# Performance work log

Measured on AMD Instinct MI355X. Metric: run time of the kernel, lower is better.

The kernel has to match this reference:

```python
import jax, jax.numpy as jnp
import numpy as np

N_NODES = 50000
N_EDGES = 800000
H_DIM = 64
N_RELS = 8
N_BASES = 2
N_LAYERS = 2


def setup_inputs() -> dict:
    key = jax.random.key(0)
    ks = jax.random.split(key, 10)
    scale = 1.0 / np.sqrt(H_DIM)
    features = jax.random.normal(ks[0], (N_NODES, H_DIM), dtype=jnp.float32)
    src = jax.random.randint(ks[1], (N_EDGES,), 0, N_NODES, dtype=jnp.int32)
    dst = jax.random.randint(ks[2], (N_EDGES,), 0, N_NODES, dtype=jnp.int32)
    etype = jax.random.randint(ks[3], (N_EDGES,), 0, N_RELS, dtype=jnp.int32)
    # basis weights V: [L, B, H, H], coefficients comp: [L, R, B]
    V = jax.random.normal(ks[4], (N_LAYERS, N_BASES, H_DIM, H_DIM), dtype=jnp.float32) * scale
    comp = jax.random.normal(ks[5], (N_LAYERS, N_RELS, N_BASES), dtype=jnp.float32)
    loop_w = jax.random.normal(ks[6], (N_LAYERS, H_DIM, H_DIM), dtype=jnp.float32) * scale
    layer_bias = jnp.zeros((N_LAYERS, H_DIM), dtype=jnp.float32)
    fc_w = jax.random.normal(ks[7], (1, N_NODES * H_DIM), dtype=jnp.float32) * (1.0 / np.sqrt(N_NODES * H_DIM))
    fc_b = jnp.zeros((1,), dtype=jnp.float32)
    return {
        "features": features, "V": V, "comp": comp, "loop_w": loop_w,
        "layer_bias": layer_bias, "fc_w": fc_w, "fc_b": fc_b,
        "src": src, "dst": dst, "etype": etype,
    }


def reference(features, V, comp, loop_w, layer_bias, fc_w, fc_b, src, dst, etype):
    N, H = features.shape
    L = V.shape[0]
    x = features
    for l in range(L):
        # basis decomposition: project nodes through each basis first (N*B*H, cheap),
        # then mix per-edge with relation coefficients -> avoids per-edge [H,H] weights
        proj = jnp.einsum('ni,bio->nbo', x, V[l])          # [N, B, H]
        msg = jnp.einsum('eb,ebo->eo', comp[l][etype], proj[src])  # [E, H]
        agg = jax.ops.segment_sum(msg, dst, num_segments=N)        # [N, H]
        h = agg + x @ loop_w[l] + layer_bias[l]
        x = jax.nn.relu(h) if l < L - 1 else h
    flat = x.reshape(1, -1)                                # [1, N*H]
    return jax.nn.sigmoid(flat @ fc_w.T + fc_b)            # [1, 1]
```

## Files before the change

### kernel.cpp

```cpp
#include <hip/hip_runtime.h>
#include <hip/hip_bf16.h>
#include <math.h>

#define N_NODES 50000
#define N_EDGES 800000
#define HDIM 64

#define NBUCKET 392
#define BSHIFT  7
#define NLOC    128
#define BCAP    3072

typedef short bf16x8 __attribute__((ext_vector_type(8)));
typedef float f32x4  __attribute__((ext_vector_type(4)));
typedef unsigned short ushort_t;

__device__ __forceinline__ ushort_t f2bf(float f) {
    __hip_bfloat16 b = __float2bfloat16(f);
    return *(ushort_t*)&b;
}
__device__ __forceinline__ void unpack8(uint4 u, float* f) {
    f[0] = __uint_as_float(u.x << 16); f[1] = __uint_as_float(u.x & 0xFFFF0000u);
    f[2] = __uint_as_float(u.y << 16); f[3] = __uint_as_float(u.y & 0xFFFF0000u);
    f[4] = __uint_as_float(u.z << 16); f[5] = __uint_as_float(u.z & 0xFFFF0000u);
    f[6] = __uint_as_float(u.w << 16); f[7] = __uint_as_float(u.w & 0xFFFF0000u);
}

__global__ __launch_bounds__(256) void prep_kernel(
    const float* __restrict__ features, ushort_t* __restrict__ x_bf,
    const float* __restrict__ V, const float* __restrict__ lw,
    ushort_t* __restrict__ Wt, int* __restrict__ bucketFill,
    float* __restrict__ scalar, int* __restrict__ done)
{
    const int b = blockIdx.x;
    const int t = threadIdx.x;
    if (b < 3125) {
        const int i = b * 256 + t;
        const float4 v = ((const float4*)features)[i];
        ushort4 o = { f2bf(v.x), f2bf(v.y), f2bf(v.z), f2bf(v.w) };
        *(ushort4*)&x_bf[(size_t)i * 4] = o;
    } else if (b < 3221) {
        const int e = (b - 3125) * 256 + t;
        const int l = e / 12288, r = e % 12288;
        const int n = r / 192, k = r % 192;
        const int sel = k >> 6, i = k & 63;
        const float val = (sel < 2) ? V[l * 8192 + sel * 4096 + i * 64 + n]
                                    : lw[l * 4096 + i * 64 + n];
        Wt[e] = f2bf(val);
    } else {
        for (int i = t; i < NBUCKET; i += 256) bucketFill[i] = 0;
        if (t == 0) { scalar[0] = 0.0f; done[0] = 0; }
    }
}

__global__ __launch_bounds__(256) void bucket_scatter(
    const int* __restrict__ src, const int* __restrict__ dst,
    const int* __restrict__ etype, int* __restrict__ bucketFill,
    unsigned int* __restrict__ buf)
{
    __shared__ int cnt[NBUCKET];
    __shared__ int base[NBUCKET];
    const int t = threadIdx.x;
    for (int i = t; i < NBUCKET; i += 256) cnt[i] = 0;
    __syncthreads();

    int rank[8], bkt[8];
    unsigned pay[8];
    bool valid[8];
#pragma unroll
    for (int k = 0; k < 8; ++k) {
        const int e = blockIdx.x * 2048 + k * 256 + t;
        valid[k] = (e < N_EDGES);
        if (valid[k]) {
            const int d = dst[e];
            const int b = d >> BSHIFT;
            bkt[k] = b;
            pay[k] = (unsigned)src[e] | ((unsigned)etype[e] << 16)
                   | ((unsigned)(d & (NLOC - 1)) << 19);
            rank[k] = atomicAdd(&cnt[b], 1);
        }
    }
    __syncthreads();
    for (int i = t; i < NBUCKET; i += 256)
        base[i] = atomicAdd(&bucketFill[i], cnt[i]);
    __syncthreads();
#pragma unroll
    for (int k = 0; k < 8; ++k) {
        if (valid[k]) {
            const int pos = base[bkt[k]] + rank[k];
            if (pos < BCAP) buf[bkt[k] * BCAP + pos] = pay[k];
        }
    }
}

__global__ __launch_bounds__(256) void bucket_sort(
    const unsigned int* __restrict__ buf, const int* __restrict__ bucketFill,
    unsigned int* __restrict__ edges, int* __restrict__ row_ptr)
{
    __shared__ int hist[NLOC];
    __shared__ int lscan[NLOC];
    __shared__ int cnt2[NLOC];
    __shared__ int sraw[448];
    __shared__ int sexc[448];
    const int b = blockIdx.x;
    const int t = threadIdx.x;

    if (t < NLOC) { hist[t] = 0; cnt2[t] = 0; }
    for (int i = t; i < 448; i += 256)
        sraw[i] = (i < NBUCKET) ? bucketFill[i] : 0;
    __syncthreads();

    if (t < 64) {
        int carry = 0;
        for (int c = 0; c < 7; ++c) {
            const int h = sraw[c * 64 + t];
            int x = h;
#pragma unroll
            for (int off = 1; off < 64; off <<= 1) {
                int u = __shfl_up(x, off, 64);
                if (t >= off) x += u;
            }
            sexc[c * 64 + t] = carry + x - h;
            carry += __shfl(x, 63, 64);
        }
    }
    __syncthreads();
    const int cntb = min(sraw[b], BCAP);
    const int bb   = sexc[b];

    for (int i0 = t; i0 < cntb; i0 += 1024) {
        const bool v1 = i0 + 256 < cntb, v2 = i0 + 512 < cntb, v3 = i0 + 768 < cntb;
        const unsigned p0 = buf[b * BCAP + i0];
        unsigned p1 = 0, p2 = 0, p3 = 0;
        if (v1) p1 = buf[b * BCAP + i0 + 256];
        if (v2) p2 = buf[b * BCAP + i0 + 512];
        if (v3) p3 = buf[b * BCAP + i0 + 768];
        atomicAdd(&hist[p0 >> 19], 1);
        if (v1) atomicAdd(&hist[p1 >> 19], 1);
        if (v2) atomicAdd(&hist[p2 >> 19], 1);
        if (v3) atomicAdd(&hist[p3 >> 19], 1);
    }
    __syncthreads();

    if (t < 64) {
        int carry = 0;
        for (int c = 0; c < 2; ++c) {
            const int h = hist[c * 64 + t];
            int x = h;
#pragma unroll
            for (int off = 1; off < 64; off <<= 1) {
                int u = __shfl_up(x, off, 64);
                if (t >= off) x += u;
            }
            lscan[c * 64 + t] = carry + x - h;
            carry += __shfl(x, 63, 64);
        }
    }
    __syncthreads();

    const int n0 = b << BSHIFT;
    if (t < NLOC) {
        const int g = n0 + t;
        if (g < N_NODES) row_ptr[g] = bb + lscan[t];
    }
    if (b == NBUCKET - 1 && t == 0) row_ptr[N_NODES] = bb + cntb;

    for (int i0 = t; i0 < cntb; i0 += 1024) {
        const bool v1 = i0 + 256 < cntb, v2 = i0 + 512 < cntb, v3 = i0 + 768 < cntb;
        const unsigned p0 = buf[b * BCAP + i0];
        unsigned p1 = 0, p2 = 0, p3 = 0;
        if (v1) p1 = buf[b * BCAP + i0 + 256];
        if (v2) p2 = buf[b * BCAP + i0 + 512];
        if (v3) p3 = buf[b * BCAP + i0 + 768];
        {
            const int d = p0 >> 19;
            const int r = atomicAdd(&cnt2[d], 1);
            edges[bb + lscan[d] + r] = p0 & 0x7FFFFu;
        }
        if (v1) { const int d = p1 >> 19; const int r = atomicAdd(&cnt2[d], 1);
                  edges[bb + lscan[d] + r] = p1 & 0x7FFFFu; }
        if (v2) { const int d = p2 >> 19; const int r = atomicAdd(&cnt2[d], 1);
                  edges[bb + lscan[d] + r] = p2 & 0x7FFFFu; }
        if (v3) { const int d = p3 >> 19; const int r = atomicAdd(&cnt2[d], 1);
                  edges[bb + lscan[d] + r] = p3 & 0x7FFFFu; }
    }
}

template <bool FUSE>
__global__ __launch_bounds__(256) void fused_layer(
    const ushort_t* __restrict__ xin,
    const unsigned int* __restrict__ edges,
    const int* __restrict__ row_ptr,
    const float* __restrict__ comp_l,
    const ushort_t* __restrict__ Wt,
    const float* __restrict__ bias,
    const float* __restrict__ fcw,
    ushort_t* __restrict__ xout,
    float* __restrict__ scalar,
    const float* __restrict__ fcb,
    int* __restrict__ done,
    float* __restrict__ outp)
{
    __shared__ __align__(16) ushort_t su[32 * 200];
    __shared__ float sred[4];
    const int t = threadIdx.x;
    const int tile = blockIdx.x;

    const int grp = t >> 3;
    const int fo  = t & 7;
    const int n   = tile * 32 + grp;

    int beg = 0, end = 0;
    if (n < N_NODES) { beg = row_ptr[n]; end = row_ptr[n + 1]; }

    float a0[8], a1[8];
#pragma unroll
    for (int i = 0; i < 8; ++i) { a0[i] = 0.f; a1[i] = 0.f; }

    for (int j = beg; j < end; j += 4) {
        unsigned pk[4];
        float2 c[4];
#pragma unroll
        for (int k = 0; k < 4; ++k) {
            const int jk = j + k;
            const unsigned p = edges[(jk < end) ? jk : (end - 1)];
            pk[k] = p;
            float2 cc = *(const float2*)&comp_l[(p >> 16) * 2];
            if (jk >= end) { cc.x = 0.f; cc.y = 0.f; }
            c[k] = cc;
        }
        uint4 u[4];
#pragma unroll
        for (int k = 0; k < 4; ++k)
            u[k] = *(const uint4*)&xin[(size_t)(pk[k] & 0xFFFFu) * 64 + fo * 8];
#pragma unroll
        for (int k = 0; k < 4; ++k) {
            float f[8];
            unpack8(u[k], f);
#pragma unroll
            for (int i = 0; i < 8; ++i) {
                a0[i] = fmaf(c[k].x, f[i], a0[i]);
                a1[i] = fmaf(c[k].y, f[i], a1[i]);
            }
        }
    }

    uint4 o0, o1;
    o0.x = (unsigned)f2bf(a0[0]) | ((unsigned)f2bf(a0[1]) << 16);
    o0.y = (unsigned)f2bf(a0[2]) | ((unsigned)f2bf(a0[3]) << 16);
    o0.z = (unsigned)f2bf(a0[4]) | ((unsigned)f2bf(a0[5]) << 16);
    o0.w = (unsigned)f2bf(a0[6]) | ((unsigned)f2bf(a0[7]) << 16);
    o1.x = (unsigned)f2bf(a1[0]) | ((unsigned)f2bf(a1[1]) << 16);
    o1.y = (unsigned)f2bf(a1[2]) | ((unsigned)f2bf(a1[3]) << 16);
    o1.z = (unsigned)f2bf(a1[4]) | ((unsigned)f2bf(a1[5]) << 16);
    o1.w = (unsigned)f2bf(a1[6]) | ((unsigned)f2bf(a1[7]) << 16);
    uint4 xt = {0u, 0u, 0u, 0u};
    if (n < N_NODES) xt = *(const uint4*)&xin[(size_t)n * 64 + fo * 8];
    *(uint4*)&su[grp * 200 + fo * 8]        = o0;
    *(uint4*)&su[grp * 200 + (8 + fo) * 8]  = o1;
    *(uint4*)&su[grp * 200 + (16 + fo) * 8] = xt;
    __syncthreads();

    const int w    = t >> 6;
    const int lane = t & 63;
    const int c16  = lane & 15;
    const int quad = lane >> 4;

    bf16x8 wf[6];
#pragma unroll
    for (int kf = 0; kf < 6; ++kf)
        wf[kf] = *(const bf16x8*)&Wt[(w * 16 + c16) * 192 + kf * 32 + quad * 8];
    const float bv = bias[w * 16 + c16];

    float fsum = 0.f;
#pragma unroll
    for (int mt = 0; mt < 2; ++mt) {
        f32x4 acc = {bv, bv, bv, bv};
#pragma unroll
        for (int kf = 0; kf < 6; ++kf) {
            const bf16x8 af =
                *(const bf16x8*)&su[(mt * 16 + c16) * 200 + kf * 32 + quad * 8];
            acc = __builtin_amdgcn_mfma_f32_16x16x32_bf16(af, wf[kf], acc, 0, 0, 0);
        }
        const int nodeb = tile * 32 + mt * 16 + quad * 4;
        if (FUSE) {
#pragma unroll
            for (int r = 0; r < 4; ++r) {
                const int nn = nodeb + r;
                if (nn < N_NODES)
                    fsum += acc[r] * fcw[(size_t)nn * 64 + w * 16 + c16];
            }
        } else {
#pragma unroll
            for (int r = 0; r < 4; ++r) {
                const int nn = nodeb + r;
                if (nn < N_NODES)
                    xout[(size_t)nn * 64 + w * 16 + c16] = f2bf(fmaxf(acc[r], 0.f));
            }
        }
    }

    if (FUSE) {
#pragma unroll
        for (int off = 32; off; off >>= 1) fsum += __shfl_down(fsum, off, 64);
        if (lane == 0) sred[w] = fsum;
        __syncthreads();
        if (t == 0) {
            atomicAdd(scalar, sred[0] + sred[1] + sred[2] + sred[3]);
            __threadfence();
            const int ticket = atomicAdd(done, 1);
            if (ticket == (int)gridDim.x - 1) {
                const float v = atomicAdd(scalar, 0.0f) + fcb[0];
                outp[0] = 1.0f / (1.0f + expf(-v));
            }
        }
    }
}

extern "C" void kernel_launch(void* const* d_in, const int* in_sizes, int n_in,
                              void* d_out, int out_size, void* d_ws, size_t ws_size,
                              hipStream_t stream)
{
    const float* features = (const float*)d_in[0];
    const float* V        = (const float*)d_in[1];
    const float* comp     = (const float*)d_in[2];
    const float* loop_w   = (const float*)d_in[3];
    const float* bias     = (const float*)d_in[4];
    const float* fc_w     = (const float*)d_in[5];
    const float* fc_b     = (const float*)d_in[6];
    const int*   src      = (const int*)d_in[7];
    const int*   dst      = (const int*)d_in[8];
    const int*   etype    = (const int*)d_in[9];
    float* out = (float*)d_out;

    char* ws = (char*)d_ws;
    ushort_t*     x_bf    = (ushort_t*)(ws);
    ushort_t*     x1_bf   = (ushort_t*)(ws + 6400000);
    ushort_t*     Wt      = (ushort_t*)(ws + 12800000);
    float*        scalar  = (float*)   (ws + 12849152);
    int*          done    = (int*)     (ws + 12849156);
    int*          bucketFill = (int*)  (ws + 12849280);
    int*          row_ptr = (int*)     (ws + 12850944);
    unsigned int* edges   = (unsigned int*)(ws + 13051008);
    unsigned int* buf     = (unsigned int*)(ws + 16251008);

    const int flBlocks = (N_NODES + 31) / 32;
    const int k1Blocks = (N_EDGES + 2047) / 2048;

    prep_kernel<<<3222, 256, 0, stream>>>(features, x_bf, V, loop_w, Wt,
                                          bucketFill, scalar, done);
    bucket_scatter<<<k1Blocks, 256, 0, stream>>>(src, dst, etype, bucketFill, buf);
    bucket_sort<<<NBUCKET, 256, 0, stream>>>(buf, bucketFill, edges, row_ptr);

    fused_layer<false><<<flBlocks, 256, 0, stream>>>(
        x_bf, edges, row_ptr, comp, Wt, bias, nullptr, x1_bf,
        nullptr, nullptr, nullptr, nullptr);

    fused_layer<true><<<flBlocks, 256, 0, stream>>>(
        x1_bf, edges, row_ptr, comp + 16, Wt + 12288, bias + 64, fc_w, nullptr,
        scalar, fc_b, done, out);
}
```

Measured before the change: 206.3 us.

## Aggregate edges per tile with wave-per-edge LDS float atomics instead of per-node loops

Replaces the per-node gather, where 8 threads walk one node's edge list, with a tile-wide edge loop. Each wave takes groups of 4 edges, each lane loads one feature, and partial sums are accumulated into an fp32 LDS buffer with atomics, using a fast path when all 4 edges share a destination. Edge records now keep the destination bits so the local slot can be recovered. This is meant to remove load imbalance from varying node degree and the serialized per-node loops. In exchange it uses scalar 2-byte loads and LDS atomic traffic, and needs extra LDS and an extra sync.

New measurement: 594.2 us. 2.88x slower.

```diff
diff --git a/kernel.cpp b/kernel.cpp
--- a/kernel.cpp
+++ b/kernel.cpp
@@ -18,12 +18,6 @@
 __device__ __forceinline__ ushort_t f2bf(float f) {
     __hip_bfloat16 b = __float2bfloat16(f);
     return *(ushort_t*)&b;
-}
-__device__ __forceinline__ void unpack8(uint4 u, float* f) {
-    f[0] = __uint_as_float(u.x << 16); f[1] = __uint_as_float(u.x & 0xFFFF0000u);
-    f[2] = __uint_as_float(u.y << 16); f[3] = __uint_as_float(u.y & 0xFFFF0000u);
-    f[4] = __uint_as_float(u.z << 16); f[5] = __uint_as_float(u.z & 0xFFFF0000u);
-    f[6] = __uint_as_float(u.w << 16); f[7] = __uint_as_float(u.w & 0xFFFF0000u);
 }
 
 __global__ __launch_bounds__(256) void prep_kernel(
@@ -175,14 +169,14 @@
         {
             const int d = p0 >> 19;
             const int r = atomicAdd(&cnt2[d], 1);
-            edges[bb + lscan[d] + r] = p0 & 0x7FFFFu;
+            edges[bb + lscan[d] + r] = p0;
         }
         if (v1) { const int d = p1 >> 19; const int r = atomicAdd(&cnt2[d], 1);
-                  edges[bb + lscan[d] + r] = p1 & 0x7FFFFu; }
+                  edges[bb + lscan[d] + r] = p1; }
         if (v2) { const int d = p2 >> 19; const int r = atomicAdd(&cnt2[d], 1);
-                  edges[bb + lscan[d] + r] = p2 & 0x7FFFFu; }
+                  edges[bb + lscan[d] + r] = p2; }
         if (v3) { const int d = p3 >> 19; const int r = atomicAdd(&cnt2[d], 1);
-                  edges[bb + lscan[d] + r] = p3 & 0x7FFFFu; }
+                  edges[bb + lscan[d] + r] = p3; }
     }
 }
 
@@ -201,76 +195,98 @@
     int* __restrict__ done,
     float* __restrict__ outp)
 {
+    __shared__ __align__(16) float    suf[32 * 128];
     __shared__ __align__(16) ushort_t su[32 * 200];
     __shared__ float sred[4];
-    const int t = threadIdx.x;
+    const int t    = threadIdx.x;
     const int tile = blockIdx.x;
-
-    const int grp = t >> 3;
-    const int fo  = t & 7;
-    const int n   = tile * 32 + grp;
-
-    int beg = 0, end = 0;
-    if (n < N_NODES) { beg = row_ptr[n]; end = row_ptr[n + 1]; }
-
-    float a0[8], a1[8];
-#pragma unroll
-    for (int i = 0; i < 8; ++i) { a0[i] = 0.f; a1[i] = 0.f; }
-
-    for (int j = beg; j < end; j += 4) {
-        unsigned pk[4];
-        float2 c[4];
-#pragma unroll
-        for (int k = 0; k < 4; ++k) {
-            const int jk = j + k;
-            const unsigned p = edges[(jk < end) ? jk : (end - 1)];
-            pk[k] = p;
-            float2 cc = *(const float2*)&comp_l[(p >> 16) * 2];
-            if (jk >= end) { cc.x = 0.f; cc.y = 0.f; }
-            c[k] = cc;
-        }
-        uint4 u[4];
-#pragma unroll
-        for (int k = 0; k < 4; ++k)
-            u[k] = *(const uint4*)&xin[(size_t)(pk[k] & 0xFFFFu) * 64 + fo * 8];
-#pragma unroll
-        for (int k = 0; k < 4; ++k) {
-            float f[8];
-            unpack8(u[k], f);
-#pragma unroll
-            for (int i = 0; i < 8; ++i) {
-                a0[i] = fmaf(c[k].x, f[i], a0[i]);
-                a1[i] = fmaf(c[k].y, f[i], a1[i]);
-            }
-        }
-    }
-
-    uint4 o0, o1;
-    o0.x = (unsigned)f2bf(a0[0]) | ((unsigned)f2bf(a0[1]) << 16);
-    o0.y = (unsigned)f2bf(a0[2]) | ((unsigned)f2bf(a0[3]) << 16);
-    o0.z = (unsigned)f2bf(a0[4]) | ((unsigned)f2bf(a0[5]) << 16);
-    o0.w = (unsigned)f2bf(a0[6]) | ((unsigned)f2bf(a0[7]) << 16);
-    o1.x = (unsigned)f2bf(a1[0]) | ((unsigned)f2bf(a1[1]) << 16);
-    o1.y = (unsigned)f2bf(a1[2]) | ((unsigned)f2bf(a1[3]) << 16);
-    o1.z = (unsigned)f2bf(a1[4]) | ((unsigned)f2bf(a1[5]) << 16);
-    o1.w = (unsigned)f2bf(a1[6]) | ((unsigned)f2bf(a1[7]) << 16);
-    uint4 xt = {0u, 0u, 0u, 0u};
-    if (n < N_NODES) xt = *(const uint4*)&xin[(size_t)n * 64 + fo * 8];
-    *(uint4*)&su[grp * 200 + fo * 8]        = o0;
-    *(uint4*)&su[grp * 200 + (8 + fo) * 8]  = o1;
-    *(uint4*)&su[grp * 200 + (16 + fo) * 8] = xt;
-    __syncthreads();
-
     const int w    = t >> 6;
     const int lane = t & 63;
     const int c16  = lane & 15;
     const int quad = lane >> 4;
+    const int grp  = t >> 3;
+    const int fo   = t & 7;
 
     bf16x8 wf[6];
 #pragma unroll
     for (int kf = 0; kf < 6; ++kf)
         wf[kf] = *(const bf16x8*)&Wt[(w * 16 + c16) * 192 + kf * 32 + quad * 8];
     const float bv = bias[w * 16 + c16];
+
+    {
+        const f32x4 z = {0.f, 0.f, 0.f, 0.f};
+        *(f32x4*)&suf[t * 16]      = z;
+        *(f32x4*)&suf[t * 16 + 4]  = z;
+        *(f32x4*)&suf[t * 16 + 8]  = z;
+        *(f32x4*)&suf[t * 16 + 12] = z;
+    }
+    {
+        const int n = tile * 32 + grp;
+        uint4 xt = {0u, 0u, 0u, 0u};
+        if (n < N_NODES) xt = *(const uint4*)&xin[(size_t)n * 64 + fo * 8];
+        *(uint4*)&su[grp * 200 + (16 + fo) * 8] = xt;
+    }
+    __syncthreads();
+
+    const int nb   = tile * 32;
+    const int nend = min(nb + 32, N_NODES);
+    const int ebeg = row_ptr[nb];
+    const int eend = row_ptr[nend];
+    const int tloc = (tile & 3) * 32;
+
+    for (int e0 = ebeg + w * 4; e0 < eend; e0 += 16) {
+        unsigned p[4];
+        float2 c[4];
+        int sl[4];
+#pragma unroll
+        for (int k = 0; k < 4; ++k) {
+            const int e = e0 + k;
+            const unsigned pp = edges[(e < eend) ? e : (eend - 1)];
+            p[k] = pp;
+            float2 cc = *(const float2*)&comp_l[((pp >> 16) & 7u) * 2];
+            if (e >= eend) { cc.x = 0.f; cc.y = 0.f; }
+            c[k] = cc;
+            sl[k] = (int)(pp >> 19) - tloc;
+        }
+        float f[4];
+#pragma unroll
+        for (int k = 0; k < 4; ++k) {
+            const ushort_t us = xin[(size_t)(p[k] & 0xFFFFu) * 64 + lane];
+            f[k] = __uint_as_float(((unsigned)us) << 16);
+        }
+        if (sl[0] == sl[1] && sl[1] == sl[2] && sl[2] == sl[3]) {
+            float s0 = c[0].x * f[0] + c[1].x * f[1] + c[2].x * f[2] + c[3].x * f[3];
+            float s1 = c[0].y * f[0] + c[1].y * f[1] + c[2].y * f[2] + c[3].y * f[3];
+            atomicAdd(&suf[sl[0] * 128 + lane], s0);
+            atomicAdd(&suf[sl[0] * 128 + 64 + lane], s1);
+        } else {
+#pragma unroll
+            for (int k = 0; k < 4; ++k) {
+                atomicAdd(&suf[sl[k] * 128 + lane], c[k].x * f[k]);
+                atomicAdd(&suf[sl[k] * 128 + 64 + lane], c[k].y * f[k]);
+            }
+        }
+    }
+    __syncthreads();
+
+    {
+        const float4 u0 = *(const float4*)&suf[grp * 128 + fo * 8];
+        const float4 u1 = *(const float4*)&suf[grp * 128 + fo * 8 + 4];
+        const float4 v0 = *(const float4*)&suf[grp * 128 + 64 + fo * 8];
+        const float4 v1 = *(const float4*)&suf[grp * 128 + 64 + fo * 8 + 4];
+        uint4 o0, o1;
+        o0.x = (unsigned)f2bf(u0.x) | ((unsigned)f2bf(u0.y) << 16);
+        o0.y = (unsigned)f2bf(u0.z) | ((unsigned)f2bf(u0.w) << 16);
+        o0.z = (unsigned)f2bf(u1.x) | ((unsigned)f2bf(u1.y) << 16);
+        o0.w = (unsigned)f2bf(u1.z) | ((unsigned)f2bf(u1.w) << 16);
+        o1.x = (unsigned)f2bf(v0.x) | ((unsigned)f2bf(v0.y) << 16);
+        o1.y = (unsigned)f2bf(v0.z) | ((unsigned)f2bf(v0.w) << 16);
+        o1.z = (unsigned)f2bf(v1.x) | ((unsigned)f2bf(v1.y) << 16);
+        o1.w = (unsigned)f2bf(v1.z) | ((unsigned)f2bf(v1.w) << 16);
+        *(uint4*)&su[grp * 200 + fo * 8]       = o0;
+        *(uint4*)&su[grp * 200 + (8 + fo) * 8] = o1;
+    }
+    __syncthreads();
 
     float fsum = 0.f;
 #pragma unroll
```

## Split fused layer into separate gather-aggregate and MFMA transform kernels

Applied to the files above, without the earlier changes.

Each layer's fused kernel becomes two kernels. The first aggregates neighbours with 16 lanes per node, reading 4 features per lane and keeping relation coefficients in shared memory, then writes the two basis-mixed sums as a bf16 buffer. The second loads that buffer plus the node's own features and runs the MFMA projection over 64-node tiles. The aim is to raise occupancy and memory parallelism in the gather-bound phase. The cost is an extra round trip of the intermediate buffer through global memory and two more kernel launches. The sorted edge array now keeps the full packed word, so the relation type is masked out with &7 at read time.

Measured after the change: 188.8 us. -8.5%, faster.

```diff
diff --git a/kernel.cpp b/kernel.cpp
--- a/kernel.cpp
+++ b/kernel.cpp
@@ -18,12 +18,6 @@
 __device__ __forceinline__ ushort_t f2bf(float f) {
     __hip_bfloat16 b = __float2bfloat16(f);
     return *(ushort_t*)&b;
-}
-__device__ __forceinline__ void unpack8(uint4 u, float* f) {
-    f[0] = __uint_as_float(u.x << 16); f[1] = __uint_as_float(u.x & 0xFFFF0000u);
-    f[2] = __uint_as_float(u.y << 16); f[3] = __uint_as_float(u.y & 0xFFFF0000u);
-    f[4] = __uint_as_float(u.z << 16); f[5] = __uint_as_float(u.z & 0xFFFF0000u);
-    f[6] = __uint_as_float(u.w << 16); f[7] = __uint_as_float(u.w & 0xFFFF0000u);
 }
 
 __global__ __launch_bounds__(256) void prep_kernel(
@@ -175,23 +169,82 @@
         {
             const int d = p0 >> 19;
             const int r = atomicAdd(&cnt2[d], 1);
-            edges[bb + lscan[d] + r] = p0 & 0x7FFFFu;
+            edges[bb + lscan[d] + r] = p0;
         }
         if (v1) { const int d = p1 >> 19; const int r = atomicAdd(&cnt2[d], 1);
-                  edges[bb + lscan[d] + r] = p1 & 0x7FFFFu; }
+                  edges[bb + lscan[d] + r] = p1; }
         if (v2) { const int d = p2 >> 19; const int r = atomicAdd(&cnt2[d], 1);
-                  edges[bb + lscan[d] + r] = p2 & 0x7FFFFu; }
+                  edges[bb + lscan[d] + r] = p2; }
         if (v3) { const int d = p3 >> 19; const int r = atomicAdd(&cnt2[d], 1);
-                  edges[bb + lscan[d] + r] = p3 & 0x7FFFFu; }
-    }
-}
-
-template <bool FUSE>
-__global__ __launch_bounds__(256) void fused_layer(
-    const ushort_t* __restrict__ xin,
+                  edges[bb + lscan[d] + r] = p3; }
+    }
+}
+
+__global__ __launch_bounds__(256) void aggregate_v4(
+    const ushort_t* __restrict__ x,
     const unsigned int* __restrict__ edges,
     const int* __restrict__ row_ptr,
     const float* __restrict__ comp_l,
+    ushort_t* __restrict__ y)
+{
+    __shared__ float scomp[16];
+    const int t = threadIdx.x;
+    if (t < 16) scomp[t] = comp_l[t];
+    __syncthreads();
+
+    const int lane = t & 63;
+    const int wv   = t >> 6;
+    const int g    = lane >> 4;
+    const int fq   = lane & 15;
+    const int n    = blockIdx.x * 16 + wv * 4 + g;
+
+    const int beg = row_ptr[n];
+    const int end = row_ptr[n + 1];
+
+    float a0[4], a1[4];
+#pragma unroll
+    for (int i = 0; i < 4; ++i) { a0[i] = 0.f; a1[i] = 0.f; }
+
+    for (int j = beg; j < end; j += 4) {
+        unsigned p[4];
+#pragma unroll
+        for (int k = 0; k < 4; ++k) {
+            const int e = j + k;
+            p[k] = edges[(e < end) ? e : (end - 1)];
+        }
+        uint2 u[4];
+#pragma unroll
+        for (int k = 0; k < 4; ++k)
+            u[k] = *(const uint2*)&x[(size_t)(p[k] & 0xFFFFu) * 64 + fq * 4];
+        float2 c[4];
+#pragma unroll
+        for (int k = 0; k < 4; ++k) {
+            c[k] = *(const float2*)&scomp[((p[k] >> 16) & 7u) * 2];
+            if (j + k >= end) { c[k].x = 0.f; c[k].y = 0.f; }
+        }
+#pragma unroll
+        for (int k = 0; k < 4; ++k) {
+            const float f0 = __uint_as_float(u[k].x << 16);
+            const float f1 = __uint_as_float(u[k].x & 0xFFFF0000u);
+            const float f2 = __uint_as_float(u[k].y << 16);
+            const float f3 = __uint_as_float(u[k].y & 0xFFFF0000u);
+            a0[0] = fmaf(c[k].x, f0, a0[0]); a1[0] = fmaf(c[k].y, f0, a1[0]);
+            a0[1] = fmaf(c[k].x, f1, a0[1]); a1[1] = fmaf(c[k].y, f1, a1[1]);
+            a0[2] = fmaf(c[k].x, f2, a0[2]); a1[2] = fmaf(c[k].y, f2, a1[2]);
+            a0[3] = fmaf(c[k].x, f3, a0[3]); a1[3] = fmaf(c[k].y, f3, a1[3]);
+        }
+    }
+
+    ushort4 s0 = { f2bf(a0[0]), f2bf(a0[1]), f2bf(a0[2]), f2bf(a0[3]) };
+    ushort4 s1 = { f2bf(a1[0]), f2bf(a1[1]), f2bf(a1[2]), f2bf(a1[3]) };
+    *(ushort4*)&y[(size_t)n * 128 + fq * 4]      = s0;
+    *(ushort4*)&y[(size_t)n * 128 + 64 + fq * 4] = s1;
+}
+
+template <bool FUSE>
+__global__ __launch_bounds__(256) void mfma_transform(
+    const ushort_t* __restrict__ y_bf,
+    const ushort_t* __restrict__ x_bf,
     const ushort_t* __restrict__ Wt,
     const float* __restrict__ bias,
     const float* __restrict__ fcw,
@@ -201,70 +254,14 @@
     int* __restrict__ done,
     float* __restrict__ outp)
 {
-    __shared__ __align__(16) ushort_t su[32 * 200];
+    __shared__ __align__(16) ushort_t su[64 * 200];
     __shared__ float sred[4];
     const int t = threadIdx.x;
+    const int w = t >> 6;
+    const int lane = t & 63;
+    const int c16 = lane & 15;
+    const int quad = lane >> 4;
     const int tile = blockIdx.x;
-
-    const int grp = t >> 3;
-    const int fo  = t & 7;
-    const int n   = tile * 32 + grp;
-
-    int beg = 0, end = 0;
-    if (n < N_NODES) { beg = row_ptr[n]; end = row_ptr[n + 1]; }
-
-    float a0[8], a1[8];
-#pragma unroll
-    for (int i = 0; i < 8; ++i) { a0[i] = 0.f; a1[i] = 0.f; }
-
-    for (int j = beg; j < end; j += 4) {
-        unsigned pk[4];
-        float2 c[4];
-#pragma unroll
-        for (int k = 0; k < 4; ++k) {
-            const int jk = j + k;
-            const unsigned p = edges[(jk < end) ? jk : (end - 1)];
-            pk[k] = p;
-            float2 cc = *(const float2*)&comp_l[(p >> 16) * 2];
-            if (jk >= end) { cc.x = 0.f; cc.y = 0.f; }
-            c[k] = cc;
-        }
-        uint4 u[4];
-#pragma unroll
-        for (int k = 0; k < 4; ++k)
-            u[k] = *(const uint4*)&xin[(size_t)(pk[k] & 0xFFFFu) * 64 + fo * 8];
-#pragma unroll
-        for (int k = 0; k < 4; ++k) {
-            float f[8];
-            unpack8(u[k], f);
-#pragma unroll
-            for (int i = 0; i < 8; ++i) {
-                a0[i] = fmaf(c[k].x, f[i], a0[i]);
-                a1[i] = fmaf(c[k].y, f[i], a1[i]);
-            }
-        }
-    }
-
-    uint4 o0, o1;
-    o0.x = (unsigned)f2bf(a0[0]) | ((unsigned)f2bf(a0[1]) << 16);
-    o0.y = (unsigned)f2bf(a0[2]) | ((unsigned)f2bf(a0[3]) << 16);
-    o0.z = (unsigned)f2bf(a0[4]) | ((unsigned)f2bf(a0[5]) << 16);
-    o0.w = (unsigned)f2bf(a0[6]) | ((unsigned)f2bf(a0[7]) << 16);
-    o1.x = (unsigned)f2bf(a1[0]) | ((unsigned)f2bf(a1[1]) << 16);
-    o1.y = (unsigned)f2bf(a1[2]) | ((unsigned)f2bf(a1[3]) << 16);
-    o1.z = (unsigned)f2bf(a1[4]) | ((unsigned)f2bf(a1[5]) << 16);
-    o1.w = (unsigned)f2bf(a1[6]) | ((unsigned)f2bf(a1[7]) << 16);
-    uint4 xt = {0u, 0u, 0u, 0u};
-    if (n < N_NODES) xt = *(const uint4*)&xin[(size_t)n * 64 + fo * 8];
-    *(uint4*)&su[grp * 200 + fo * 8]        = o0;
-    *(uint4*)&su[grp * 200 + (8 + fo) * 8]  = o1;
-    *(uint4*)&su[grp * 200 + (16 + fo) * 8] = xt;
-    __syncthreads();
-
-    const int w    = t >> 6;
-    const int lane = t & 63;
-    const int c16  = lane & 15;
-    const int quad = lane >> 4;
 
     bf16x8 wf[6];
 #pragma unroll
@@ -272,9 +269,24 @@
         wf[kf] = *(const bf16x8*)&Wt[(w * 16 + c16) * 192 + kf * 32 + quad * 8];
     const float bv = bias[w * 16 + c16];
 
+#pragma unroll
+    for (int k = 0; k < 6; ++k) {
+        const int cid = t + 256 * k;
+        const int row = cid / 24;
+        const int part = cid % 24;
+        const int n = tile * 64 + row;
+        uint4 v = {0u, 0u, 0u, 0u};
+        if (n < N_NODES) {
+            v = (part < 16) ? *(const uint4*)&y_bf[(size_t)n * 128 + part * 8]
+                            : *(const uint4*)&x_bf[(size_t)n * 64 + (part - 16) * 8];
+        }
+        *(uint4*)&su[row * 200 + part * 8] = v;
+    }
+    __syncthreads();
+
     float fsum = 0.f;
 #pragma unroll
-    for (int mt = 0; mt < 2; ++mt) {
+    for (int mt = 0; mt < 4; ++mt) {
         f32x4 acc = {bv, bv, bv, bv};
 #pragma unroll
         for (int kf = 0; kf < 6; ++kf) {
@@ -282,20 +294,20 @@
                 *(const bf16x8*)&su[(mt * 16 + c16) * 200 + kf * 32 + quad * 8];
             acc = __builtin_amdgcn_mfma_f32_16x16x32_bf16(af, wf[kf], acc, 0, 0, 0);
         }
-        const int nodeb = tile * 32 + mt * 16 + quad * 4;
+        const int nodeb = tile * 64 + mt * 16 + quad * 4;
         if (FUSE) {
 #pragma unroll
             for (int r = 0; r < 4; ++r) {
-                const int nn = nodeb + r;
-                if (nn < N_NODES)
-                    fsum += acc[r] * fcw[(size_t)nn * 64 + w * 16 + c16];
+                const int n = nodeb + r;
+                if (n < N_NODES)
+                    fsum += acc[r] * fcw[(size_t)n * 64 + w * 16 + c16];
             }
         } else {
 #pragma unroll
             for (int r = 0; r < 4; ++r) {
-                const int nn = nodeb + r;
-                if (nn < N_NODES)
-                    xout[(size_t)nn * 64 + w * 16 + c16] = f2bf(fmaxf(acc[r], 0.f));
+                const int n = nodeb + r;
+                if (n < N_NODES)
+                    xout[(size_t)n * 64 + w * 16 + c16] = f2bf(fmaxf(acc[r], 0.f));
             }
         }
     }
@@ -334,29 +346,31 @@
     float* out = (float*)d_out;
 
     char* ws = (char*)d_ws;
-    ushort_t*     x_bf    = (ushort_t*)(ws);
-    ushort_t*     x1_bf   = (ushort_t*)(ws + 6400000);
-    ushort_t*     Wt      = (ushort_t*)(ws + 12800000);
-    float*        scalar  = (float*)   (ws + 12849152);
-    int*          done    = (int*)     (ws + 12849156);
-    int*          bucketFill = (int*)  (ws + 12849280);
-    int*          row_ptr = (int*)     (ws + 12850944);
-    unsigned int* edges   = (unsigned int*)(ws + 13051008);
-    unsigned int* buf     = (unsigned int*)(ws + 16251008);
-
-    const int flBlocks = (N_NODES + 31) / 32;
-    const int k1Blocks = (N_EDGES + 2047) / 2048;
+    ushort_t*     y_bf    = (ushort_t*)(ws);
+    ushort_t*     x_bf    = (ushort_t*)(ws + 12800000);
+    ushort_t*     x1_bf   = (ushort_t*)(ws + 19200000);
+    ushort_t*     Wt      = (ushort_t*)(ws + 25600000);
+    float*        scalar  = (float*)   (ws + 25649152);
+    int*          done    = (int*)     (ws + 25649156);
+    int*          bucketFill = (int*)  (ws + 25649280);
+    int*          row_ptr = (int*)     (ws + 25650944);
+    unsigned int* edges   = (unsigned int*)(ws + 25851008);
+    unsigned int* buf     = (unsigned int*)(ws + 29051008);
+
+    const int aggBlocks = N_NODES / 16;
+    const int mtBlocks  = (N_NODES + 63) / 64;
+    const int k1Blocks  = (N_EDGES + 2047) / 2048;
 
     prep_kernel<<<3222, 256, 0, stream>>>(features, x_bf, V, loop_w, Wt,
                                           bucketFill, scalar, done);
     bucket_scatter<<<k1Blocks, 256, 0, stream>>>(src, dst, etype, bucketFill, buf);
     bucket_sort<<<NBUCKET, 256, 0, stream>>>(buf, bucketFill, edges, row_ptr);
 
-    fused_layer<false><<<flBlocks, 256, 0, stream>>>(
-        x_bf, edges, row_ptr, comp, Wt, bias, nullptr, x1_bf,
-        nullptr, nullptr, nullptr, nullptr);
-
-    fused_layer<true><<<flBlocks, 256, 0, stream>>>(
-        x1_bf, edges, row_ptr, comp + 16, Wt + 12288, bias + 64, fc_w, nullptr,
-        scalar, fc_b, done, out);
-}
+    aggregate_v4<<<aggBlocks, 256, 0, stream>>>(x_bf, edges, row_ptr, comp, y_bf);
+    mfma_transform<false><<<mtBlocks, 256, 0, stream>>>(
+        y_bf, x_bf, Wt, bias, nullptr, x1_bf, nullptr, nullptr, nullptr, nullptr);
+
+    aggregate_v4<<<aggBlocks, 256, 0, stream>>>(x1_bf, edges, row_ptr, comp + 16, y_bf);
+    mfma_transform<true><<<mtBlocks, 256, 0, stream>>>(
+        y_bf, x1_bf, Wt + 12288, bias + 64, fc_w, nullptr, scalar, fc_b, done, out);
+}
```
